# Optimization experiments

Measured on AMD Instinct MI355X. Metric: run time of the kernel, lower is better.

Reference implementation:

```python
import jax, jax.numpy as jnp
import numpy as np

B, S, HID = 1, 2048, 4096
NH, NKV = 32, 8
HD = HID // NH            # 128
GROUPS = NH // NKV        # 4
ROPE_THETA = 10000.0


def _rope_cos_sin(seq_len, head_dim, dtype=jnp.float32):
    inv_freq = 1.0 / (ROPE_THETA ** (jnp.arange(0, head_dim, 2, dtype=jnp.float32) / head_dim))
    t = jnp.arange(seq_len, dtype=jnp.float32)
    freqs = jnp.outer(t, inv_freq)                      # [S, HD/2]
    emb = jnp.concatenate([freqs, freqs], axis=-1)      # [S, HD]
    return jnp.cos(emb).astype(dtype), jnp.sin(emb).astype(dtype)


def _rotate_half(x):
    x1, x2 = jnp.split(x, 2, axis=-1)
    return jnp.concatenate([-x2, x1], axis=-1)


def _apply_rope(x, cos, sin):
    # x: [B, H, S, HD]; cos/sin: [S, HD] (position_ids = arange(S), no past)
    return x * cos[None, None] + _rotate_half(x) * sin[None, None]


def setup_inputs() -> dict:
    key = jax.random.key(0)
    k1, k2, k3, k4, k5 = jax.random.split(key, 5)
    return {
        "hidden_states": jax.random.normal(k1, (B, S, HID), jnp.float32),
        "Wq": jax.random.normal(k2, (NH * HD, HID), jnp.float32) * 0.02,
        "Wk": jax.random.normal(k3, (NKV * HD, HID), jnp.float32) * 0.02,
        "Wv": jax.random.normal(k4, (NKV * HD, HID), jnp.float32) * 0.02,
        "Wo": jax.random.normal(k5, (HID, NH * HD), jnp.float32) * 0.02,
    }


def reference(hidden_states, Wq, Wk, Wv, Wo):
    bsz, q_len, _ = hidden_states.shape
    # projections (nn.Linear: x @ W.T)
    q = (hidden_states @ Wq.T).reshape(bsz, q_len, NH, HD).transpose(0, 2, 1, 3)   # [B,NH,S,HD]
    k = (hidden_states @ Wk.T).reshape(bsz, q_len, NKV, HD).transpose(0, 2, 1, 3)  # [B,NKV,S,HD]
    v = (hidden_states @ Wv.T).reshape(bsz, q_len, NKV, HD).transpose(0, 2, 1, 3)

    cos, sin = _rope_cos_sin(q_len, HD, hidden_states.dtype)
    q = _apply_rope(q, cos, sin)
    k = _apply_rope(k, cos, sin)

    # GQA: repeat kv heads (repeat_kv / num_key_value_groups)
    k = jnp.repeat(k, GROUPS, axis=1)   # [B,NH,S,HD]
    v = jnp.repeat(v, GROUPS, axis=1)

    scale = 1.0 / jnp.sqrt(jnp.asarray(HD, hidden_states.dtype))
    logits = jnp.einsum('bhqd,bhkd->bhqk', q, k) * scale   # [B,NH,S,S]

    # prefill causal mask (phys_past_len = 0)
    causal = jnp.tril(jnp.ones((q_len, q_len), dtype=bool))
    logits = jnp.where(causal[None, None], logits, jnp.finfo(logits.dtype).min)

    attn = jax.nn.softmax(logits, axis=-1)
    out = jnp.einsum('bhqk,bhkd->bhqd', attn, v)            # [B,NH,S,HD]
    out = out.transpose(0, 2, 1, 3).reshape(bsz, q_len, NH * HD)
    return out @ Wo.T
```

## Files before the change

### kernel.cpp

```cpp
#include <hip/hip_runtime.h>

typedef __bf16 bf16;
typedef __bf16 bf16x2 __attribute__((ext_vector_type(2)));
typedef __bf16 bf16x4 __attribute__((ext_vector_type(4)));
typedef __bf16 bf16x8 __attribute__((ext_vector_type(8)));
typedef float f32x4 __attribute__((ext_vector_type(4)));

#define S_LEN 2048
#define HID_DIM 4096
#define NH 32
#define NKV 8
#define HD 128
#define QKV_N 6144
#define K_COL 4096
#define V_COL 5120
#define PADV 76

__global__ void cvt_all_kernel(const float* __restrict__ hs, const float* __restrict__ wq,
                               const float* __restrict__ wk, const float* __restrict__ wv,
                               const float* __restrict__ wo, bf16* __restrict__ hsb,
                               bf16* __restrict__ wqkvb, bf16* __restrict__ wob,
                               float* __restrict__ cost, float* __restrict__ sint) {
  long i = (long)blockIdx.x * blockDim.x + threadIdx.x;
  if (i >= 12582912) {
    int j = (int)(i - 12582912);
    int s = j >> 6, d = j & 63;
    float inv = expf(-0.14391156831212787f * (float)d);
    float ang = (float)s * inv;
    cost[j] = cosf(ang);
    sint[j] = sinf(ang);
    return;
  }
  const float* src; bf16* dst; long off;
  if (i < 2097152)      { src = hs; dst = hsb;                          off = i; }
  else if (i < 6291456) { src = wq; dst = wqkvb;                        off = i - 2097152; }
  else if (i < 7340032) { src = wk; dst = wqkvb + (long)4096 * 4096;    off = i - 6291456; }
  else if (i < 8388608) { src = wv; dst = wqkvb + (long)5120 * 4096;    off = i - 7340032; }
  else                  { src = wo; dst = wob;                          off = i - 8388608; }
  float4 v = reinterpret_cast<const float4*>(src)[off];
  bf16x4 o;
  o[0] = (bf16)v.x; o[1] = (bf16)v.y; o[2] = (bf16)v.z; o[3] = (bf16)v.w;
  reinterpret_cast<bf16x4*>(dst)[off] = o;
}

__global__ void rope_apply_kernel(bf16* __restrict__ qkv, const float* __restrict__ cost,
                                  const float* __restrict__ sint) {
  int idx = blockIdx.x * blockDim.x + threadIdx.x;
  int s = idx / 320;
  int c = idx - s * 320;
  int g = c >> 3, dc = (c & 7) * 8;
  long base = (long)s * QKV_N + g * 128 + dc;
  bf16x8 x1 = *reinterpret_cast<const bf16x8*>(qkv + base);
  bf16x8 x2 = *reinterpret_cast<const bf16x8*>(qkv + base + 64);
  const float* cp = cost + (s << 6) + dc;
  const float* sp = sint + (s << 6) + dc;
  float4 ca = *reinterpret_cast<const float4*>(cp);
  float4 cb = *reinterpret_cast<const float4*>(cp + 4);
  float4 sa = *reinterpret_cast<const float4*>(sp);
  float4 sb = *reinterpret_cast<const float4*>(sp + 4);
  float co[8] = {ca.x, ca.y, ca.z, ca.w, cb.x, cb.y, cb.z, cb.w};
  float sn[8] = {sa.x, sa.y, sa.z, sa.w, sb.x, sb.y, sb.z, sb.w};
  bf16x8 y1, y2;
#pragma unroll
  for (int e = 0; e < 8; ++e) {
    float a = (float)x1[e], b = (float)x2[e];
    y1[e] = (bf16)(a * co[e] - b * sn[e]);
    y2[e] = (bf16)(b * co[e] + a * sn[e]);
  }
  *reinterpret_cast<bf16x8*>(qkv + base)      = y1;
  *reinterpret_cast<bf16x8*>(qkv + base + 64) = y2;
}

#define STG8(buf, mat, kt, unit) {                                                       \
    const bf16* sp_ = (mat) ? Bp : Ap;                                                   \
    int row0_ = ((mat) ? n0 : m0) + (unit) * 64;                                         \
    int lb_ = (buf) * LBUF + (mat) * 16384 + (unit) * 4096;                              \
    int r_ = t >> 3, jl_ = t & 7, jg_ = jl_ ^ (r_ & 7);                                  \
    const bf16* src_ = sp_ + (long)(row0_ + r_) * K + (kt) * 64 + jg_ * 8;               \
    __builtin_amdgcn_global_load_lds((const __attribute__((address_space(1))) void*)src_,\
        (__attribute__((address_space(3))) void*)(L + lb_ + t * 8), 16, 0, 0); }

#define DSA2(buf, mh) {                                                                  \
    _Pragma("unroll") for (int ks_ = 0; ks_ < 2; ++ks_)                                  \
      _Pragma("unroll") for (int mf_ = 0; mf_ < 4; ++mf_) {                              \
        int R_ = wr * 128 + (mh) * 64 + mf_ * 16 + lm;                                   \
        aF[ks_][mf_] = *reinterpret_cast<const bf16x8*>(                                 \
            L + (buf) * LBUF + R_ * 64 + (((ks_ * 4 + lg) ^ (R_ & 7)) << 3));            \
      } }

#define DSBALL(buf) {                                                                    \
    _Pragma("unroll") for (int ks_ = 0; ks_ < 2; ++ks_)                                  \
      _Pragma("unroll") for (int nf_ = 0; nf_ < NB; ++nf_) {                             \
        int R_ = wc * (NB * 16) + nf_ * 16 + lm;                                         \
        bF[ks_][nf_] = *reinterpret_cast<const bf16x8*>(                                 \
            L + (buf) * LBUF + 16384 + R_ * 64 + (((ks_ * 4 + lg) ^ (R_ & 7)) << 3));    \
      } }

#define MM2(mh) {                                                                        \
    __builtin_amdgcn_s_setprio(1);                                                       \
    _Pragma("unroll") for (int mf_ = 0; mf_ < 4; ++mf_)                                  \
      _Pragma("unroll") for (int nf_ = 0; nf_ < NB; ++nf_)                               \
        _Pragma("unroll") for (int ks_ = 0; ks_ < 2; ++ks_)                              \
          acc[(mh) * 4 + mf_][nf_] = __builtin_amdgcn_mfma_f32_16x16x32_bf16(            \
              aF[ks_][mf_], bF[ks_][nf_], acc[(mh) * 4 + mf_][nf_], 0, 0, 0);            \
    __builtin_amdgcn_s_setprio(0); }

#define BAR() __builtin_amdgcn_s_barrier()
#define WVM(n) asm volatile("s_waitcnt vmcnt(%0)" :: "i"(n) : "memory")

template<int NB, typename OutT>
__global__ __launch_bounds__(512, 1) void gemm4p_kernel(
    const bf16* __restrict__ Ap, const bf16* __restrict__ Bp, OutT* __restrict__ C,
    int M, int N, int K) {
  constexpr int LBUF = 16384 + NB * 4096;
  __shared__ __align__(16) bf16 L[2 * LBUF];

  int nwg = gridDim.x * gridDim.y;
  int bid = blockIdx.y * gridDim.x + blockIdx.x;
  int cpx = nwg >> 3;
  int swz = (bid & 7) * cpx + (bid >> 3);
  int bxs = swz % gridDim.x, bys = swz / gridDim.x;
  const int n0 = bxs * (NB * 64), m0 = bys * 256;

  const int t = threadIdx.x;
  const int lane = t & 63, w = t >> 6;
  const int wr = w >> 2, wc = w & 3;
  const int lg = lane >> 4, lm = lane & 15;
  const int NT = K >> 6;

  f32x4 acc[8][NB] = {};
  bf16x8 aF[2][4], bF[2][NB];

  STG8(0, 0, 0, 0); STG8(0, 0, 0, 1); STG8(0, 0, 0, 2); STG8(0, 0, 0, 3);
  STG8(0, 1, 0, 0); if (NB > 1) STG8(0, 1, 0, 1); if (NB > 2) STG8(0, 1, 0, 2);
  STG8(1, 1, 1, 0); if (NB > 1) STG8(1, 1, 1, 1); if (NB > 2) STG8(1, 1, 1, 2);
  WVM(NB);
  BAR();

  for (int I = 0; I < (NT >> 1); ++I) {
    const int tt = 2 * I;
    const bool pf = (I < (NT >> 1) - 1);
    DSA2(0, 0); DSBALL(0);
    STG8(1, 0, tt + 1, 0); STG8(1, 0, tt + 1, 1);
    STG8(1, 0, tt + 1, 2); STG8(1, 0, tt + 1, 3);
    BAR(); MM2(0); BAR();
    DSA2(0, 1);
    if (pf) { STG8(0, 1, tt + 2, 0); if (NB > 1) STG8(0, 1, tt + 2, 1);
              if (NB > 2) STG8(0, 1, tt + 2, 2); }
    BAR(); MM2(1);
    if (pf) WVM(NB); else WVM(0);
    BAR();
    DSA2(1, 0); DSBALL(1);
    if (pf) { STG8(0, 0, tt + 2, 0); STG8(0, 0, tt + 2, 1);
              STG8(0, 0, tt + 2, 2); STG8(0, 0, tt + 2, 3); }
    BAR(); MM2(0); BAR();
    DSA2(1, 1);
    if (pf) { STG8(1, 1, tt + 3, 0); if (NB > 1) STG8(1, 1, tt + 3, 1);
              if (NB > 2) STG8(1, 1, tt + 3, 2); }
    BAR(); MM2(1);
    if (pf) WVM(NB); else WVM(0);
    BAR();
  }

#pragma unroll
  for (int am = 0; am < 8; ++am) {
    int row = m0 + wr * 128 + am * 16 + lg * 4;
#pragma unroll
    for (int nf = 0; nf < NB; ++nf) {
      int col = n0 + wc * (NB * 16) + nf * 16 + lm;
#pragma unroll
      for (int rr = 0; rr < 4; ++rr) {
        if constexpr (sizeof(OutT) == 4) C[(long)(row + rr) * N + col] = acc[am][nf][rr];
        else                             C[(long)(row + rr) * N + col] = (bf16)acc[am][nf][rr];
      }
    }
  }
}

#define AK_LBAR() { asm volatile("s_waitcnt lgkmcnt(0)" ::: "memory");                   \
                    __builtin_amdgcn_s_barrier(); }
#define AK_VBAR() { asm volatile("s_waitcnt vmcnt(4)" ::: "memory");                     \
                    __builtin_amdgcn_sched_barrier(0);                                   \
                    asm volatile("s_waitcnt lgkmcnt(0)" ::: "memory");                   \
                    __builtin_amdgcn_s_barrier(); }

#define AK_WRITEV(r0, r1) {                                                              \
    _Pragma("unroll") for (int e = 0; e < 8; ++e) {                                      \
      bf16x2 pk; pk[0] = r0[e]; pk[1] = r1[e];                                           \
      *reinterpret_cast<bf16x2*>(Vt + (dchunk * 8 + e) * PADV + slot) = pk;              \
    } }

#define AK_ISSUEV(base, r0, r1) {                                                        \
    long rv_ = (long)(base) + kva; if (rv_ > 2046) rv_ = 2046;                           \
    const bf16* vs_ = vbase + rv_ * QKV_N + dchunk * 8;                                  \
    r0 = *reinterpret_cast<const bf16x8*>(vs_);                                          \
    r1 = *reinterpret_cast<const bf16x8*>(vs_ + QKV_N); }

#define AK_ISSUEK(base, buf) {                                                           \
    _Pragma("unroll") for (int i_ = 0; i_ < 2; ++i_) {                                   \
      int c_ = i_ * 512 + t;                                                             \
      int r_ = c_ >> 4, jl_ = c_ & 15, jg_ = jl_ ^ (r_ & 15);                            \
      long rk_ = (long)(base) + r_; if (rk_ > 2047) rk_ = 2047;                          \
      const bf16* src_ = kbase + rk_ * QKV_N + jg_ * 8;                                  \
      __builtin_amdgcn_global_load_lds((const __attribute__((address_space(1))) void*)src_,\
          (__attribute__((address_space(3))) void*)(Ks[buf] + c_ * 8), 16, 0, 0);        \
    } }

#define AK_STEP(stv, ksb) {                                                              \
    const int st_ = (stv);                                                               \
    const int kv0_ = st_ * 64;                                                           \
    if (kv0_ <= q0 + w * 16 + 15) {                                                      \
      f32x4 s[4];                                                                        \
      _Pragma("unroll") for (int cb = 0; cb < 4; ++cb) s[cb] = f32x4{0.f,0.f,0.f,0.f};   \
      __builtin_amdgcn_s_setprio(1);                                                     \
      _Pragma("unroll") for (int ks = 0; ks < 4; ++ks)                                   \
        _Pragma("unroll") for (int cb = 0; cb < 4; ++cb) {                               \
          bf16x8 kf = *reinterpret_cast<const bf16x8*>(                                  \
              Ks[ksb] + (cb * 16 + lm) * 128 + (((ks * 4 + lg) ^ lm) << 3));             \
          s[cb] = __builtin_amdgcn_mfma_f32_16x16x32_bf16(kf, qf[ks], s[cb], 0, 0, 0);   \
        }                                                                                \
      __builtin_amdgcn_s_setprio(0);                                                     \
      const float SC = 0.12751742f;                                                      \
      float sl[4][4];                                                                    \
      _Pragma("unroll") for (int cb = 0; cb < 4; ++cb)                                   \
        _Pragma("unroll") for (int r = 0; r < 4; ++r) {                                  \
          float v = s[cb][r] * SC;                                                       \
          if (st_ >= nst - 2 && (kv0_ + cb * 16 + lg * 4 + r) > qg) v = -1e30f;          \
          sl[cb][r] = v;                                                                 \
        }                                                                                \
      float tm = sl[0][0];                                                               \
      _Pragma("unroll") for (int cb = 0; cb < 4; ++cb)                                   \
        _Pragma("unroll") for (int r = 0; r < 4; ++r) tm = fmaxf(tm, sl[cb][r]);         \
      tm = fmaxf(tm, __shfl_xor(tm, 16));                                                \
      tm = fmaxf(tm, __shfl_xor(tm, 32));                                                \
      if (__any(tm > mrow + 8.f)) {                                                      \
        float mnew = fmaxf(mrow, tm);                                                    \
        float alpha = exp2f(mrow - mnew);                                                \
        mrow = mnew; lrow *= alpha;                                                      \
        float ar[4];                                                                     \
        _Pragma("unroll") for (int r = 0; r < 4; ++r)                                    \
          ar[r] = __shfl(alpha, (lane & 48) | (lg * 4 + r));                             \
        _Pragma("unroll") for (int i = 0; i < 8; ++i)                                    \
          _Pragma("unroll") for (int r = 0; r < 4; ++r) o[i][r] *= ar[r];                \
      }                                                                                  \
      float p[4][4]; float psum = 0.f;                                                   \
      _Pragma("unroll") for (int cb = 0; cb < 4; ++cb)                                   \
        _Pragma("unroll") for (int r = 0; r < 4; ++r) {                                  \
          p[cb][r] = exp2f(sl[cb][r] - mrow); psum += p[cb][r];                          \
        }                                                                                \
      psum += __shfl_xor(psum, 16);                                                      \
      psum += __shfl_xor(psum, 32);                                                      \
      lrow += psum;                                                                      \
      bf16x8 pa0, pa1;                                                                   \
      _Pragma("unroll") for (int r = 0; r < 4; ++r) {                                    \
        pa0[r] = (bf16)p[0][r]; pa0[4 + r] = (bf16)p[1][r];                              \
        pa1[r] = (bf16)p[2][r]; pa1[4 + r] = (bf16)p[3][r];                              \
      }                                                                                  \
      __builtin_amdgcn_s_setprio(1);                                                     \
      _Pragma("unroll") for (int db = 0; db < 8; ++db) {                                 \
        bf16x8 vf0 = *reinterpret_cast<const bf16x8*>(Vt + (db*16+lm)*PADV + lg*8);      \
        bf16x8 vf1 = *reinterpret_cast<const bf16x8*>(Vt + (db*16+lm)*PADV + 32 + lg*8); \
        o[db] = __builtin_amdgcn_mfma_f32_16x16x32_bf16(pa0, vf0, o[db], 0, 0, 0);       \
        o[db] = __builtin_amdgcn_mfma_f32_16x16x32_bf16(pa1, vf1, o[db], 0, 0, 0);       \
      }                                                                                  \
      __builtin_amdgcn_s_setprio(0);                                                     \
    } }

__global__ __launch_bounds__(512, 4) void attn_kernel(const bf16* __restrict__ qkv,
                                                      bf16* __restrict__ out) {
  __shared__ __align__(16) bf16 Ks[2][64 * 128];
  __shared__ __align__(16) bf16 Vt[128 * PADV];

  const int bx = blockIdx.x;
  const int qt = 15 - (bx >> 5);
  const int h = bx & 31;
  const int kvh = h >> 2;
  const int q0 = qt * 128;
  const int t = threadIdx.x, lane = t & 63, w = t >> 6;
  const int lg = lane >> 4, lm = lane & 15;
  const int dchunk = t >> 5, kv2 = t & 31;
  const int kva = kv2 * 2;
  const int k5 = kva & 31;
  const int slot = ((kva >> 5) << 5) | (((k5 >> 2) & 3) << 3) | ((k5 >> 4) << 2) | (k5 & 3);
  const bf16* kbase = qkv + K_COL + kvh * HD;
  const bf16* vbase = qkv + V_COL + kvh * HD;

  const long qrow = q0 + w * 16 + lm;
  const int qg = q0 + w * 16 + lm;
  bf16x8 qf[4];
#pragma unroll
  for (int ks = 0; ks < 4; ++ks)
    qf[ks] = *reinterpret_cast<const bf16x8*>(qkv + qrow * QKV_N + h * HD + ks * 32 + lg * 8);

  f32x4 o[8];
#pragma unroll
  for (int i = 0; i < 8; ++i) o[i] = f32x4{0.f, 0.f, 0.f, 0.f};
  float mrow = -1e30f, lrow = 0.f;

  const int nst = 2 * qt + 2;
  bf16x8 va0, va1, vb0, vb1;

  AK_ISSUEV(0, va0, va1);
  AK_ISSUEK(0, 0);
  AK_ISSUEV(64, vb0, vb1);
  AK_ISSUEK(64, 1);
  AK_WRITEV(va0, va1);
  AK_VBAR();

  for (int I = 0; I < (nst >> 1); ++I) {
    const int s0 = 2 * I;
    AK_STEP(s0, 0);
    AK_LBAR();
    AK_WRITEV(vb0, vb1);
    AK_ISSUEV((s0 + 2) * 64, va0, va1);
    AK_ISSUEK((s0 + 2) * 64, 0);
    AK_VBAR();
    AK_STEP(s0 + 1, 1);
    AK_LBAR();
    AK_WRITEV(va0, va1);
    AK_ISSUEV((s0 + 3) * 64, vb0, vb1);
    AK_ISSUEK((s0 + 3) * 64, 1);
    AK_VBAR();
  }

  float invr[4];
#pragma unroll
  for (int r = 0; r < 4; ++r)
    invr[r] = 1.0f / __shfl(lrow, (lane & 48) | (lg * 4 + r));
#pragma unroll
  for (int r = 0; r < 4; ++r) {
    long row = q0 + w * 16 + lg * 4 + r;
#pragma unroll
    for (int db = 0; db < 8; ++db)
      out[row * HID_DIM + h * HD + db * 16 + lm] = (bf16)(o[db][r] * invr[r]);
  }
}

extern "C" void kernel_launch(void* const* d_in, const int* in_sizes, int n_in,
                              void* d_out, int out_size, void* d_ws, size_t ws_size,
                              hipStream_t stream) {
  const float* hs = (const float*)d_in[0];
  const float* Wq = (const float*)d_in[1];
  const float* Wk = (const float*)d_in[2];
  const float* Wv = (const float*)d_in[3];
  const float* Wo = (const float*)d_in[4];
  float* out = (float*)d_out;
  char* ws = (char*)d_ws;

  bf16*  hsb   = (bf16*)(ws);
  bf16*  wqkvb = (bf16*)(ws + 16777216);
  bf16*  wob   = (bf16*)(ws + 67108864);
  bf16*  qkv   = (bf16*)(ws + 100663296);
  bf16*  attn  = (bf16*)(ws + 125829120);
  float* cost  = (float*)(ws + 142606336);
  float* sint  = (float*)(ws + 143130624);

  cvt_all_kernel<<<49664, 256, 0, stream>>>(hs, Wq, Wk, Wv, Wo, hsb, wqkvb, wob, cost, sint);
  gemm4p_kernel<3, bf16><<<dim3(32, 8), 512, 0, stream>>>(hsb, wqkvb, qkv, 2048, 6144, 4096);
  rope_apply_kernel<<<2560, 256, 0, stream>>>(qkv, cost, sint);
  attn_kernel<<<512, 512, 0, stream>>>(qkv, attn);
  gemm4p_kernel<2, float><<<dim3(32, 8), 512, 0, stream>>>(attn, wob, out, 2048, 4096, 4096);
}
```

Before: 302.5 us.

## Double-buffer V tile in LDS and cut attention loop to one barrier per step

The V tile in shared memory is now double-buffered, matching the already double-buffered K tiles. The attention main loop is reordered so each step issues the next K and V loads and writes the previously loaded V registers into the spare buffer before computing. This allows a single barrier per KV step instead of two, removing synchronisation stalls between the QK and PV phases. The cost is more shared memory per block, roughly 71KB instead of 51KB, which may reduce how many blocks fit on a CU.

```diff
diff --git a/kernel.cpp b/kernel.cpp
--- a/kernel.cpp
+++ b/kernel.cpp
@@ -177,17 +177,15 @@
   }
 }
 
-#define AK_LBAR() { asm volatile("s_waitcnt lgkmcnt(0)" ::: "memory");                   \
-                    __builtin_amdgcn_s_barrier(); }
-#define AK_VBAR() { asm volatile("s_waitcnt vmcnt(4)" ::: "memory");                     \
-                    __builtin_amdgcn_sched_barrier(0);                                   \
-                    asm volatile("s_waitcnt lgkmcnt(0)" ::: "memory");                   \
-                    __builtin_amdgcn_s_barrier(); }
-
-#define AK_WRITEV(r0, r1) {                                                              \
+#define AK_BAR() { asm volatile("s_waitcnt vmcnt(2)" ::: "memory");                      \
+                   __builtin_amdgcn_sched_barrier(0);                                    \
+                   asm volatile("s_waitcnt lgkmcnt(0)" ::: "memory");                    \
+                   __builtin_amdgcn_s_barrier(); }
+
+#define AK_WRITEV(r0, r1, vtb) {                                                         \
     _Pragma("unroll") for (int e = 0; e < 8; ++e) {                                      \
       bf16x2 pk; pk[0] = r0[e]; pk[1] = r1[e];                                           \
-      *reinterpret_cast<bf16x2*>(Vt + (dchunk * 8 + e) * PADV + slot) = pk;              \
+      *reinterpret_cast<bf16x2*>(Vt[vtb] + (dchunk * 8 + e) * PADV + slot) = pk;         \
     } }
 
 #define AK_ISSUEV(base, r0, r1) {                                                        \
@@ -206,7 +204,7 @@
           (__attribute__((address_space(3))) void*)(Ks[buf] + c_ * 8), 16, 0, 0);        \
     } }
 
-#define AK_STEP(stv, ksb) {                                                              \
+#define AK_STEP(stv, bufb) {                                                             \
     const int st_ = (stv);                                                               \
     const int kv0_ = st_ * 64;                                                           \
     if (kv0_ <= q0 + w * 16 + 15) {                                                      \
@@ -216,7 +214,7 @@
       _Pragma("unroll") for (int ks = 0; ks < 4; ++ks)                                   \
         _Pragma("unroll") for (int cb = 0; cb < 4; ++cb) {                               \
           bf16x8 kf = *reinterpret_cast<const bf16x8*>(                                  \
-              Ks[ksb] + (cb * 16 + lm) * 128 + (((ks * 4 + lg) ^ lm) << 3));             \
+              Ks[bufb] + (cb * 16 + lm) * 128 + (((ks * 4 + lg) ^ lm) << 3));            \
           s[cb] = __builtin_amdgcn_mfma_f32_16x16x32_bf16(kf, qf[ks], s[cb], 0, 0, 0);   \
         }                                                                                \
       __builtin_amdgcn_s_setprio(0);                                                     \
@@ -258,8 +256,8 @@
       }                                                                                  \
       __builtin_amdgcn_s_setprio(1);                                                     \
       _Pragma("unroll") for (int db = 0; db < 8; ++db) {                                 \
-        bf16x8 vf0 = *reinterpret_cast<const bf16x8*>(Vt + (db*16+lm)*PADV + lg*8);      \
-        bf16x8 vf1 = *reinterpret_cast<const bf16x8*>(Vt + (db*16+lm)*PADV + 32 + lg*8); \
+        bf16x8 vf0 = *reinterpret_cast<const bf16x8*>(Vt[bufb] + (db*16+lm)*PADV + lg*8);\
+        bf16x8 vf1 = *reinterpret_cast<const bf16x8*>(Vt[bufb] + (db*16+lm)*PADV + 32 + lg*8);\
         o[db] = __builtin_amdgcn_mfma_f32_16x16x32_bf16(pa0, vf0, o[db], 0, 0, 0);       \
         o[db] = __builtin_amdgcn_mfma_f32_16x16x32_bf16(pa1, vf1, o[db], 0, 0, 0);       \
       }                                                                                  \
@@ -269,7 +267,7 @@
 __global__ __launch_bounds__(512, 4) void attn_kernel(const bf16* __restrict__ qkv,
                                                       bf16* __restrict__ out) {
   __shared__ __align__(16) bf16 Ks[2][64 * 128];
-  __shared__ __align__(16) bf16 Vt[128 * PADV];
+  __shared__ __align__(16) bf16 Vt[2][128 * PADV];
 
   const int bx = blockIdx.x;
   const int qt = 15 - (bx >> 5);
@@ -300,27 +298,25 @@
   const int nst = 2 * qt + 2;
   bf16x8 va0, va1, vb0, vb1;
 
+  AK_ISSUEK(0, 0);
   AK_ISSUEV(0, va0, va1);
-  AK_ISSUEK(0, 0);
+  AK_WRITEV(va0, va1, 0);
   AK_ISSUEV(64, vb0, vb1);
-  AK_ISSUEK(64, 1);
-  AK_WRITEV(va0, va1);
-  AK_VBAR();
+  asm volatile("s_waitcnt lgkmcnt(0)" ::: "memory");
+  __builtin_amdgcn_s_barrier();
 
   for (int I = 0; I < (nst >> 1); ++I) {
     const int s0 = 2 * I;
+    AK_ISSUEK((s0 + 1) * 64, 1);
+    AK_ISSUEV((s0 + 2) * 64, va0, va1);
+    AK_WRITEV(vb0, vb1, 1);
     AK_STEP(s0, 0);
-    AK_LBAR();
-    AK_WRITEV(vb0, vb1);
-    AK_ISSUEV((s0 + 2) * 64, va0, va1);
+    AK_BAR();
     AK_ISSUEK((s0 + 2) * 64, 0);
-    AK_VBAR();
+    AK_ISSUEV((s0 + 3) * 64, vb0, vb1);
+    AK_WRITEV(va0, va1, 0);
     AK_STEP(s0 + 1, 1);
-    AK_LBAR();
-    AK_WRITEV(va0, va1);
-    AK_ISSUEV((s0 + 3) * 64, vb0, vb1);
-    AK_ISSUEK((s0 + 3) * 64, 1);
-    AK_VBAR();
+    AK_BAR();
   }
 
   float invr[4];
```

Measured after the change: 304.3 us. No clear change (+0.6%).
